# Performance work log

Hardware: AMD Instinct MI355X
Metric: run time of the kernel (lower is better)

## Reference

```python
import jax, jax.numpy as jnp
import numpy as np

WS = 8       # window size
NH = 8       # num heads (c_=256 -> head_dim=32)
BN_EPS = 1e-5
LN_EPS = 1e-5


def _rel_pos_index(ws):
    coords = np.stack(np.meshgrid(np.arange(ws), np.arange(ws), indexing='ij')).reshape(2, -1)
    rel = (coords[:, :, None] - coords[:, None, :]).transpose(1, 2, 0)
    rel[:, :, 0] += ws - 1
    rel[:, :, 1] += ws - 1
    rel[:, :, 0] *= 2 * ws - 1
    return rel.sum(-1)  # (ws*ws, ws*ws) int

RPI = _rel_pos_index(WS)


def _attn_mask(H, W, ws, shift):
    # SW-MSA attention mask, computed from static shapes (numpy)
    img = np.zeros((H, W))
    cnt = 0
    for h in (slice(0, -ws), slice(-ws, -shift), slice(-shift, None)):
        for w in (slice(0, -ws), slice(-ws, -shift), slice(-shift, None)):
            img[h, w] = cnt
            cnt += 1
    mw = img.reshape(H // ws, ws, W // ws, ws).transpose(0, 2, 1, 3).reshape(-1, ws * ws)
    m = mw[:, None, :] - mw[:, :, None]
    return jnp.asarray(np.where(m != 0, -100.0, 0.0).astype(np.float32))  # (nW, N, N)


def _cbs(x, w, bn):
    # 1x1 conv (bias=False) + BatchNorm2d(eval) + SiLU; x:(B,Cin,H,W), w:(Cout,Cin,1,1)
    y = jnp.einsum('bchw,oc->bohw', x, w[:, :, 0, 0])
    g, b, mu, var = bn
    s = g / jnp.sqrt(var + BN_EPS)
    y = y * s[None, :, None, None] + (b - mu * s)[None, :, None, None]
    return y * jax.nn.sigmoid(y)


def _ln(x, g, b):
    mu = x.mean(-1, keepdims=True)
    var = ((x - mu) ** 2).mean(-1, keepdims=True)
    return (x - mu) / jnp.sqrt(var + LN_EPS) * g + b


def _window_attn(x, mask, qkvw, qkvb, pw, pb, rpb):
    B_, N, C = x.shape
    hd = C // NH
    qkv = (x @ qkvw.T + qkvb).reshape(B_, N, 3, NH, hd).transpose(2, 0, 3, 1, 4)
    q, k, v = qkv[0] * (hd ** -0.5), qkv[1], qkv[2]
    attn = jnp.einsum('bhnd,bhmd->bhnm', q, k)  # (B_, NH, N, N)
    bias = rpb[RPI.reshape(-1)].reshape(N, N, NH).transpose(2, 0, 1)
    attn = attn + bias[None]
    if mask is not None:
        nW = mask.shape[0]
        attn = (attn.reshape(B_ // nW, nW, NH, N, N) + mask[None, :, None]).reshape(B_, NH, N, N)
    attn = jax.nn.softmax(attn, axis=-1)
    out = jnp.einsum('bhnm,bhmd->bhnd', attn, v).transpose(0, 2, 1, 3).reshape(B_, N, C)
    return out @ pw.T + pb


def _swin_layer(x, shift, n1g, n1b, qkvw, qkvb, pw, pb, rpb, n2g, n2b, f1w, f1b, f2w, f2b):
    B, C, H, W = x.shape  # H, W divisible by WS (no pad branch)
    shortcut = x.transpose(0, 2, 3, 1).reshape(B, H * W, C)
    xn = _ln(shortcut, n1g, n1b).reshape(B, H, W, C)
    if shift > 0:
        xn = jnp.roll(xn, (-shift, -shift), axis=(1, 2))
        mask = _attn_mask(H, W, WS, shift)
    else:
        mask = None
    nh, nw = H // WS, W // WS
    xw = xn.reshape(B, nh, WS, nw, WS, C).transpose(0, 1, 3, 2, 4, 5).reshape(-1, WS * WS, C)
    aw = _window_attn(xw, mask, qkvw, qkvb, pw, pb, rpb)
    xr = aw.reshape(B, nh, nw, WS, WS, C).transpose(0, 1, 3, 2, 4, 5).reshape(B, H, W, C)
    if shift > 0:
        xr = jnp.roll(xr, (shift, shift), axis=(1, 2))
    x1 = shortcut + xr.reshape(B, H * W, C)
    h = jax.nn.gelu(_ln(x1, n2g, n2b) @ f1w.T + f1b, approximate=False)
    x2 = x1 + (h @ f2w.T + f2b)
    return x2.reshape(B, H, W, C).transpose(0, 3, 1, 2)


def setup_inputs() -> dict:
    key = jax.random.key(0)
    ks = iter(jax.random.split(key, 48))
    C1, C2, C_, NL = 512, 512, 256, 2

    def randn(shape, s=0.02):
        return jax.random.normal(next(ks), shape, jnp.float32) * s

    def bn(c):
        g = jax.random.uniform(next(ks), (c,), jnp.float32, 0.5, 1.5)
        b = randn((c,), 0.1)
        mu = randn((c,), 0.1)
        var = jax.random.uniform(next(ks), (c,), jnp.float32, 0.5, 1.5)
        return jnp.stack([g, b, mu, var])

    return dict(
        x=jax.random.normal(next(ks), (16, C1, 64, 64), jnp.float32),
        cv1_w=randn((C_, C1, 1, 1)), cv1_bn=bn(C_),
        cv2_w=randn((C_, C1, 1, 1)), cv2_bn=bn(C_),
        cv3_w=randn((C2, 2 * C_, 1, 1)), cv3_bn=bn(C2),
        norm1_g=jnp.ones((NL, C_)), norm1_b=jnp.zeros((NL, C_)),
        qkv_w=randn((NL, 3 * C_, C_)), qkv_b=jnp.zeros((NL, 3 * C_)),
        proj_w=randn((NL, C_, C_)), proj_b=jnp.zeros((NL, C_)),
        rpb=randn((NL, (2 * WS - 1) ** 2, NH)),
        norm2_g=jnp.ones((NL, C_)), norm2_b=jnp.zeros((NL, C_)),
        fc1_w=randn((NL, 4 * C_, C_)), fc1_b=jnp.zeros((NL, 4 * C_)),
        fc2_w=randn((NL, C_, 4 * C_)), fc2_b=jnp.zeros((NL, C_)),
    )


def reference(x, cv1_w, cv1_bn, cv2_w, cv2_bn, cv3_w, cv3_bn,
              norm1_g, norm1_b, qkv_w, qkv_b, proj_w, proj_b, rpb,
              norm2_g, norm2_b, fc1_w, fc1_b, fc2_w, fc2_b):
    y = _cbs(x, cv1_w, cv1_bn)
    for i in range(qkv_w.shape[0]):  # n swin layers (alternating W-MSA / SW-MSA)
        shift = 0 if i % 2 == 0 else WS // 2
        y = _swin_layer(y, shift, norm1_g[i], norm1_b[i], qkv_w[i], qkv_b[i],
                        proj_w[i], proj_b[i], rpb[i], norm2_g[i], norm2_b[i],
                        fc1_w[i], fc1_b[i], fc2_w[i], fc2_b[i])
    y2 = _cbs(x, cv2_w, cv2_bn)
    return _cbs(jnp.concatenate([y, y2], axis=1), cv3_w, cv3_bn)
```

## Files before the change

### kernel.cpp

```cpp
#include <hip/hip_runtime.h>
#include <math.h>

using bf16x8 = __attribute__((ext_vector_type(8))) short;
using f32x4  = __attribute__((ext_vector_type(4))) float;
typedef unsigned short u16;

#define DI __device__ __forceinline__

DI u16 f2bf(float f){
  union { float f; unsigned u; } v; v.f = f;
  return (u16)((v.u + 0x7fffu + ((v.u >> 16) & 1u)) >> 16);
}

DI void gll16(const void* g, void* l){
  __builtin_amdgcn_global_load_lds((const __attribute__((address_space(1))) void*)g,
                                   (__attribute__((address_space(3))) void*)l, 16, 0, 0);
}

__global__ void k_cvt(const float* __restrict__ in, u16* __restrict__ out, int n4){
  int i = blockIdx.x * 256 + threadIdx.x;
  if (i >= n4) return;
  float4 v = ((const float4*)in)[i];
  short4 o;
  o.x = (short)f2bf(v.x); o.y = (short)f2bf(v.y);
  o.z = (short)f2bf(v.z); o.w = (short)f2bf(v.w);
  ((short4*)out)[i] = o;
}

__global__ void k_xpose(const float* __restrict__ x, u16* __restrict__ xT){
  __shared__ float tile[64][65];
  int hw0 = blockIdx.x * 64, c0 = blockIdx.y * 64, b = blockIdx.z;
  int tid = threadIdx.x;
  const float* src = x + ((size_t)(b * 512 + c0)) * 4096 + hw0;
  for (int rep = 0; rep < 16; rep++){
    int idx = rep * 256 + tid;
    int cc = idx >> 6, th = idx & 63;
    tile[cc][th] = src[(size_t)cc * 4096 + th];
  }
  __syncthreads();
  u16* dst = xT + ((size_t)(b * 4096 + hw0)) * 512 + c0;
  for (int rep = 0; rep < 16; rep++){
    int idx = rep * 256 + tid;
    int tt = idx >> 6, cc = idx & 63;
    dst[(size_t)tt * 512 + cc] = f2bf(tile[cc][tt]);
  }
}

__global__ void k_ln(const float* __restrict__ xin, const float* __restrict__ g,
                     const float* __restrict__ bta, u16* __restrict__ out){
  int t = blockIdx.x * 4 + (threadIdx.x >> 6);
  int lane = threadIdx.x & 63;
  float4 v = ((const float4*)(xin + (size_t)t * 256))[lane];
  float s  = v.x + v.y + v.z + v.w;
  float s2 = v.x*v.x + v.y*v.y + v.z*v.z + v.w*v.w;
  for (int m = 1; m < 64; m <<= 1){ s += __shfl_xor(s, m, 64); s2 += __shfl_xor(s2, m, 64); }
  float mu  = s * (1.0f/256.0f);
  float var = s2 * (1.0f/256.0f) - mu*mu;
  float inv = rsqrtf(var + 1e-5f);
  float4 gg = ((const float4*)g)[lane];
  float4 bb = ((const float4*)bta)[lane];
  short4 o;
  o.x = (short)f2bf((v.x - mu) * inv * gg.x + bb.x);
  o.y = (short)f2bf((v.y - mu) * inv * gg.y + bb.y);
  o.z = (short)f2bf((v.z - mu) * inv * gg.z + bb.z);
  o.w = (short)f2bf((v.w - mu) * inv * gg.w + bb.w);
  ((short4*)(out + (size_t)t * 256))[lane] = o;
}

struct GemmP {
  const u16* A; const u16* A2; const u16* W;
  int K; int N;
  const float* bias;
  int bnN;
  const float* resid; int ldR;
  float* outF; int ldF;
  u16* outB; int ldB; int colB;
};

template<int MODE>
__launch_bounds__(256)
__global__ void k_gemm(GemmP p){
  __shared__ __align__(16) u16 sA[128 * 64];
  __shared__ __align__(16) u16 sB[128 * 64];
  __shared__ float sT[(MODE == 6) ? 32 * 136 : 1];
  int tid = threadIdx.x;
  int wave = tid >> 6, lane = tid & 63;
  int fq = lane >> 4, fr = lane & 15;
  int m0 = blockIdx.x * 128, n0 = blockIdx.y * 128;
  int wm = (wave >> 1) * 64, wn = (wave & 1) * 64;
  const int K = p.K;

  int rsub = lane >> 3;
  int gk   = ((lane & 7) ^ rsub) << 3;

  f32x4 acc[4][4];
  f32x4 z4 = {0.f, 0.f, 0.f, 0.f};
  #pragma unroll
  for (int i = 0; i < 4; i++)
    #pragma unroll
    for (int j = 0; j < 4; j++) acc[i][j] = z4;

  for (int k0 = 0; k0 < K; k0 += 64){
    #pragma unroll
    for (int it = 0; it < 4; it++){
      int row = (it * 4 + wave) * 8 + rsub;
      const u16* ga;
      if constexpr (MODE == 6){
        const u16* base = (k0 < 256) ? p.A : p.A2;
        ga = base + (size_t)(m0 + row) * 256 + (k0 & 255) + gk;
      } else {
        ga = p.A + (size_t)(m0 + row) * K + k0 + gk;
      }
      gll16(ga, sA + (it * 4 + wave) * 512);
      const u16* gb = p.W + (size_t)(n0 + row) * K + k0 + gk;
      gll16(gb, sB + (it * 4 + wave) * 512);
    }
    __syncthreads();
    #pragma unroll
    for (int kk = 0; kk < 2; kk++){
      bf16x8 af[4], bfr[4];
      #pragma unroll
      for (int i = 0; i < 4; i++){
        int r = wm + i * 16 + fr;
        af[i] = *(const bf16x8*)(sA + r * 64 + ((((kk << 2) + fq) ^ (fr & 7)) << 3));
      }
      #pragma unroll
      for (int j = 0; j < 4; j++){
        int r = wn + j * 16 + fr;
        bfr[j] = *(const bf16x8*)(sB + r * 64 + ((((kk << 2) + fq) ^ (fr & 7)) << 3));
      }
      #pragma unroll
      for (int i = 0; i < 4; i++)
        #pragma unroll
        for (int j = 0; j < 4; j++)
          acc[i][j] = __builtin_amdgcn_mfma_f32_16x16x32_bf16(af[i], bfr[j], acc[i][j], 0, 0, 0);
    }
    __syncthreads();
  }

  if constexpr (MODE != 6){
    #pragma unroll
    for (int j = 0; j < 4; j++){
      int col = n0 + wn + j * 16 + fr;
      float sc = 0.f, sh = 0.f;
      if constexpr (MODE == 0 || MODE == 1){
        float gg = p.bias[col];
        float bb = p.bias[p.bnN + col];
        float mv = p.bias[2 * p.bnN + col];
        float vv = p.bias[3 * p.bnN + col];
        sc = gg * rsqrtf(vv + 1e-5f);
        sh = bb - mv * sc;
      } else {
        sh = p.bias[col];
      }
      #pragma unroll
      for (int i = 0; i < 4; i++){
        #pragma unroll
        for (int rr = 0; rr < 4; rr++){
          int row = m0 + wm + i * 16 + fq * 4 + rr;
          float v = acc[i][j][rr];
          if constexpr (MODE == 0 || MODE == 1){ v = v * sc + sh; v = v / (1.f + __expf(-v)); }
          else v += sh;
          if constexpr (MODE == 3 || MODE == 5) v += p.resid[(size_t)row * p.ldR + col];
          if constexpr (MODE == 4) v = 0.5f * v * (1.f + erff(v * 0.70710678118f));
          if constexpr (MODE == 0 || MODE == 3 || MODE == 5) p.outF[(size_t)row * p.ldF + col] = v;
          if constexpr (MODE == 1 || MODE == 2 || MODE == 4 || MODE == 5)
            p.outB[(size_t)row * p.ldB + p.colB + col] = f2bf(v);
        }
      }
    }
  } else {
    int b = m0 >> 12;
    int hw0 = m0 & 4095;
    #pragma unroll
    for (int ps = 0; ps < 4; ps++){
      if (wn == (ps >> 1) * 64){
        #pragma unroll
        for (int jj = 0; jj < 2; jj++){
          int j = (ps & 1) * 2 + jj;
          int col = n0 + wn + j * 16 + fr;
          float gg = p.bias[col];
          float bb = p.bias[p.bnN + col];
          float mv = p.bias[2 * p.bnN + col];
          float vv = p.bias[3 * p.bnN + col];
          float sc = gg * rsqrtf(vv + 1e-5f);
          float sh = bb - mv * sc;
          int nl = wn + j * 16 + fr - ps * 32;
          #pragma unroll
          for (int i = 0; i < 4; i++)
            #pragma unroll
            for (int rr = 0; rr < 4; rr++){
              float v = acc[i][j][rr];
              v = v * sc + sh; v = v / (1.f + __expf(-v));
              sT[nl * 136 + wm + i * 16 + fq * 4 + rr] = v;
            }
        }
      }
      __syncthreads();
      for (int rep = 0; rep < 16; rep++){
        int flat = rep * 256 + tid;
        int nl = flat >> 7, ml = flat & 127;
        int c = n0 + ps * 32 + nl;
        p.outF[((size_t)(b * 512 + c)) * 4096 + hw0 + ml] = sT[nl * 136 + ml];
      }
      __syncthreads();
    }
  }
}

template<int SHIFT>
__launch_bounds__(256)
__global__ void k_attn(const u16* __restrict__ qkv, const float* __restrict__ rpb,
                       u16* __restrict__ out){
  __shared__ int tmap[64];
  __shared__ float bias_s[1800];
  __shared__ __align__(16) u16 p_s[4][64][72];
  __shared__ __align__(16) u16 vT_s[4][32][72];
  int tid = threadIdx.x, wave = tid >> 6, lane = tid & 63;
  int fq = lane >> 4, fr = lane & 15;
  int wi = blockIdx.x;
  int b = wi >> 6, wh = (wi >> 3) & 7, ww = wi & 7;

  for (int i = tid; i < 1800; i += 256) bias_s[i] = rpb[i];
  if (tid < 64){
    int r = tid >> 3, c = tid & 7;
    int h = (wh * 8 + r + SHIFT) & 63;
    int w = (ww * 8 + c + SHIFT) & 63;
    tmap[tid] = (b << 12) | (h << 6) | w;
  }
  __syncthreads();

  const float scl = 0.17677669529663687f;
  for (int hh = 0; hh < 2; hh++){
    int head = wave * 2 + hh;

    {
      const u16* vrow = qkv + (size_t)tmap[lane] * 768 + 512 + head * 32;
      #pragma unroll
      for (int cg = 0; cg < 4; cg++){
        bf16x8 vv = *(const bf16x8*)(vrow + cg * 8);
        #pragma unroll
        for (int e = 0; e < 8; e++) vT_s[wave][cg * 8 + e][lane] = (u16)vv[e];
      }
    }

    bf16x8 qf[4], kf[4];
    #pragma unroll
    for (int i = 0; i < 4; i++){
      int n = i * 16 + fr;
      size_t base = (size_t)tmap[n] * 768 + head * 32 + fq * 8;
      qf[i] = *(const bf16x8*)(qkv + base);
      kf[i] = *(const bf16x8*)(qkv + base + 256);
    }
    f32x4 z4 = {0.f, 0.f, 0.f, 0.f};
    f32x4 sfr[4][4];
    #pragma unroll
    for (int i = 0; i < 4; i++)
      #pragma unroll
      for (int j = 0; j < 4; j++) sfr[i][j] = z4;
    #pragma unroll
    for (int i = 0; i < 4; i++)
      #pragma unroll
      for (int j = 0; j < 4; j++)
        sfr[i][j] = __builtin_amdgcn_mfma_f32_16x16x32_bf16(qf[i], kf[j], sfr[i][j], 0, 0, 0);

    #pragma unroll
    for (int i = 0; i < 4; i++){
      #pragma unroll
      for (int rr = 0; rr < 4; rr++){
        int rq = i * 16 + fq * 4 + rr;
        int prq = rq >> 3, pcq = rq & 7;
        int idq = 0;
        if (SHIFT > 0){
          int rh = (wh == 7) ? ((prq >= 4) ? 2 : 1) : 0;
          int rw = (ww == 7) ? ((pcq >= 4) ? 2 : 1) : 0;
          idq = rh * 3 + rw;
        }
        float vv[4];
        float mx = -1e30f;
        #pragma unroll
        for (int j = 0; j < 4; j++){
          int m = j * 16 + fr;
          int prk = m >> 3, pck = m & 7;
          float bi = bias_s[((prq - prk + 7) * 15 + (pcq - pck + 7)) * 8 + head];
          float v = sfr[i][j][rr] * scl + bi;
          if (SHIFT > 0){
            int rhk = (wh == 7) ? ((prk >= 4) ? 2 : 1) : 0;
            int rwk = (ww == 7) ? ((pck >= 4) ? 2 : 1) : 0;
            if (idq != rhk * 3 + rwk) v -= 100.f;
          }
          vv[j] = v;
          mx = fmaxf(mx, v);
        }
        for (int mm = 1; mm < 16; mm <<= 1) mx = fmaxf(mx, __shfl_xor(mx, mm, 64));
        float sum = 0.f;
        #pragma unroll
        for (int j = 0; j < 4; j++){ vv[j] = __expf(vv[j] - mx); sum += vv[j]; }
        for (int mm = 1; mm < 16; mm <<= 1) sum += __shfl_xor(sum, mm, 64);
        float inv = 1.0f / sum;
        #pragma unroll
        for (int j = 0; j < 4; j++) p_s[wave][rq][j * 16 + fr] = f2bf(vv[j] * inv);
      }
    }
    __syncthreads();

    f32x4 o[4][2];
    #pragma unroll
    for (int i = 0; i < 4; i++){ o[i][0] = z4; o[i][1] = z4; }
    #pragma unroll
    for (int ks = 0; ks < 2; ks++){
      bf16x8 pa[4], vb[2];
      #pragma unroll
      for (int i = 0; i < 4; i++) pa[i] = *(const bf16x8*)&p_s[wave][i * 16 + fr][ks * 32 + fq * 8];
      #pragma unroll
      for (int j = 0; j < 2; j++) vb[j] = *(const bf16x8*)&vT_s[wave][j * 16 + fr][ks * 32 + fq * 8];
      #pragma unroll
      for (int i = 0; i < 4; i++)
        #pragma unroll
        for (int j = 0; j < 2; j++)
          o[i][j] = __builtin_amdgcn_mfma_f32_16x16x32_bf16(pa[i], vb[j], o[i][j], 0, 0, 0);
    }
    #pragma unroll
    for (int i = 0; i < 4; i++)
      #pragma unroll
      for (int j = 0; j < 2; j++)
        #pragma unroll
        for (int rr = 0; rr < 4; rr++){
          int rq = i * 16 + fq * 4 + rr;
          int t = tmap[rq];
          out[(size_t)t * 256 + head * 32 + j * 16 + fr] = f2bf(o[i][j][rr]);
        }
    __syncthreads();
  }
}

extern "C" void kernel_launch(void* const* d_in, const int* in_sizes, int n_in,
                              void* d_out, int out_size, void* d_ws, size_t ws_size,
                              hipStream_t stream){
  (void)in_sizes; (void)n_in; (void)out_size; (void)ws_size;
  const float* x      = (const float*)d_in[0];
  const float* cv1_w  = (const float*)d_in[1];
  const float* cv1_bn = (const float*)d_in[2];
  const float* cv2_w  = (const float*)d_in[3];
  const float* cv2_bn = (const float*)d_in[4];
  const float* cv3_w  = (const float*)d_in[5];
  const float* cv3_bn = (const float*)d_in[6];
  const float* n1g = (const float*)d_in[7];
  const float* n1b = (const float*)d_in[8];
  const float* qkvw = (const float*)d_in[9];
  const float* qkvb = (const float*)d_in[10];
  const float* pw  = (const float*)d_in[11];
  const float* pb  = (const float*)d_in[12];
  const float* rpb = (const float*)d_in[13];
  const float* n2g = (const float*)d_in[14];
  const float* n2b = (const float*)d_in[15];
  const float* f1w = (const float*)d_in[16];
  const float* f1b = (const float*)d_in[17];
  const float* f2w = (const float*)d_in[18];
  const float* f2b = (const float*)d_in[19];

  char* ws = (char*)d_ws;
  const size_t MB = 1024 * 1024;
  u16*   xT   = (u16*)(ws);
  u16*   ln_o = (u16*)(ws);
  u16*   yF   = (u16*)(ws);
  u16*   at_o = (u16*)(ws + 32 * MB);
  u16*   qkvB = (u16*)(ws + 64 * MB);
  u16*   hB   = qkvB;
  float* yS   = (float*)(ws + 192 * MB);
  float* x1   = (float*)(ws + 256 * MB);
  u16*   wp   = (u16*)(ws + 320 * MB);
  u16*   y2   = (u16*)(ws + 328 * MB);

  u16* wCv1 = wp;
  u16* wCv2 = wp + 131072;
  u16* wCv3 = wp + 262144;
  u16* wQkv = wp + 524288;
  u16* wPrj = wp + 917504;
  u16* wF1  = wp + 1048576;
  u16* wF2  = wp + 1572864;

  auto cvt = [&](const float* src, u16* dst, int n){
    int n4 = n >> 2;
    k_cvt<<<(n4 + 255) / 256, 256, 0, stream>>>(src, dst, n4);
  };
  cvt(cv1_w, wCv1, 131072);
  cvt(cv2_w, wCv2, 131072);
  cvt(cv3_w, wCv3, 262144);
  cvt(qkvw,  wQkv, 393216);
  cvt(pw,    wPrj, 131072);
  cvt(f1w,   wF1,  524288);
  cvt(f2w,   wF2,  524288);

  k_xpose<<<dim3(64, 8, 16), 256, 0, stream>>>(x, xT);

  const int M = 65536;
  auto gemm = [&](int mode, const u16* A, const u16* A2, const u16* W, int K, int N,
                  const float* bias, int bnN, const float* resid, int ldR,
                  float* outF, int ldF, u16* outB, int ldB, int colB){
    GemmP p{A, A2, W, K, N, bias, bnN, resid, ldR, outF, ldF, outB, ldB, colB};
    dim3 g(M / 128, N / 128);
    switch (mode){
      case 0: k_gemm<0><<<g, 256, 0, stream>>>(p); break;
      case 1: k_gemm<1><<<g, 256, 0, stream>>>(p); break;
      case 2: k_gemm<2><<<g, 256, 0, stream>>>(p); break;
      case 3: k_gemm<3><<<g, 256, 0, stream>>>(p); break;
      case 4: k_gemm<4><<<g, 256, 0, stream>>>(p); break;
      case 5: k_gemm<5><<<g, 256, 0, stream>>>(p); break;
      case 6: k_gemm<6><<<g, 256, 0, stream>>>(p); break;
    }
  };

  gemm(0, xT, nullptr, wCv1, 512, 256, cv1_bn, 256, nullptr, 0, yS, 256, nullptr, 0, 0);
  gemm(1, xT, nullptr, wCv2, 512, 256, cv2_bn, 256, nullptr, 0, nullptr, 0, y2, 256, 0);

  for (int l = 0; l < 2; l++){
    k_ln<<<16384, 256, 0, stream>>>(yS, n1g + l * 256, n1b + l * 256, ln_o);
    gemm(2, ln_o, nullptr, wQkv + l * 196608, 256, 768, qkvb + l * 768, 0, nullptr, 0,
         nullptr, 0, qkvB, 768, 0);
    if (l == 0) k_attn<0><<<1024, 256, 0, stream>>>(qkvB, rpb, at_o);
    else        k_attn<4><<<1024, 256, 0, stream>>>(qkvB, rpb + 1800, at_o);
    gemm(3, at_o, nullptr, wPrj + l * 65536, 256, 256, pb + l * 256, 0, yS, 256,
         x1, 256, nullptr, 0, 0);
    k_ln<<<16384, 256, 0, stream>>>(x1, n2g + l * 256, n2b + l * 256, ln_o);
    gemm(4, ln_o, nullptr, wF1 + l * 262144, 256, 1024, f1b + l * 1024, 0, nullptr, 0,
         nullptr, 0, hB, 1024, 0);
    if (l == 0)
      gemm(3, hB, nullptr, wF2 + l * 262144, 1024, 256, f2b + l * 256, 0, x1, 256,
           yS, 256, nullptr, 0, 0);
    else
      gemm(5, hB, nullptr, wF2 + l * 262144, 1024, 256, f2b + l * 256, 0, x1, 256,
           yS, 256, yF, 256, 0);
  }

  gemm(6, yF, y2, wCv3, 512, 512, cv3_bn, 512, nullptr, 0,
       (float*)d_out, 0, nullptr, 0, 0);
}
```

Measured before the change: 1.409 ms.

## Double-buffer GEMM LDS tiles and remap workgroups across XCDs

The GEMM kernel now uses two LDS buffers, so the next K-tile's global loads are issued while MFMAs run on the current tile. Explicit vmcnt waits and raw barriers replace __syncthreads. The 2D grid becomes a 1D grid with an XCD-aware block-id remap that places neighbouring tiles on the same XCD for L2 reuse. This doubles LDS use (64KB per block), which may lower occupancy.

```diff
diff --git a/kernel.cpp b/kernel.cpp
--- a/kernel.cpp
+++ b/kernel.cpp
@@ -69,7 +69,7 @@
 
 struct GemmP {
   const u16* A; const u16* A2; const u16* W;
-  int K; int N;
+  int K; int N; int NB;
   const float* bias;
   int bnN;
   const float* resid; int ldR;
@@ -80,27 +80,25 @@
 template<int MODE>
 __launch_bounds__(256)
 __global__ void k_gemm(GemmP p){
-  __shared__ __align__(16) u16 sA[128 * 64];
-  __shared__ __align__(16) u16 sB[128 * 64];
+  __shared__ __align__(16) u16 sA[2][128 * 64];
+  __shared__ __align__(16) u16 sB[2][128 * 64];
   __shared__ float sT[(MODE == 6) ? 32 * 136 : 1];
   int tid = threadIdx.x;
   int wave = tid >> 6, lane = tid & 63;
   int fq = lane >> 4, fr = lane & 15;
-  int m0 = blockIdx.x * 128, n0 = blockIdx.y * 128;
+
+  int nwg = gridDim.x;
+  int bid = blockIdx.x;
+  int lid = (bid & 7) * (nwg >> 3) + (bid >> 3);
+  int m0 = (lid / p.NB) * 128, n0 = (lid % p.NB) * 128;
+
   int wm = (wave >> 1) * 64, wn = (wave & 1) * 64;
   const int K = p.K;
 
   int rsub = lane >> 3;
   int gk   = ((lane & 7) ^ rsub) << 3;
 
-  f32x4 acc[4][4];
-  f32x4 z4 = {0.f, 0.f, 0.f, 0.f};
-  #pragma unroll
-  for (int i = 0; i < 4; i++)
-    #pragma unroll
-    for (int j = 0; j < 4; j++) acc[i][j] = z4;
-
-  for (int k0 = 0; k0 < K; k0 += 64){
+  auto STAGE = [&](int k0, int c){
     #pragma unroll
     for (int it = 0; it < 4; it++){
       int row = (it * 4 + wave) * 8 + rsub;
@@ -111,23 +109,38 @@
       } else {
         ga = p.A + (size_t)(m0 + row) * K + k0 + gk;
       }
-      gll16(ga, sA + (it * 4 + wave) * 512);
-      const u16* gb = p.W + (size_t)(n0 + row) * K + k0 + gk;
-      gll16(gb, sB + (it * 4 + wave) * 512);
-    }
-    __syncthreads();
+      gll16(ga, &sA[c][(it * 4 + wave) * 512]);
+      gll16(p.W + (size_t)(n0 + row) * K + k0 + gk, &sB[c][(it * 4 + wave) * 512]);
+    }
+  };
+
+  f32x4 acc[4][4];
+  f32x4 z4 = {0.f, 0.f, 0.f, 0.f};
+  #pragma unroll
+  for (int i = 0; i < 4; i++)
+    #pragma unroll
+    for (int j = 0; j < 4; j++) acc[i][j] = z4;
+
+  STAGE(0, 0);
+  int c = 0;
+  for (int k0 = 0; k0 < K; k0 += 64){
+    bool last = (k0 + 64 >= K);
+    if (!last) STAGE(k0 + 64, c ^ 1);
+    if (last) asm volatile("s_waitcnt vmcnt(0)" ::: "memory");
+    else      asm volatile("s_waitcnt vmcnt(8)" ::: "memory");
+    __builtin_amdgcn_s_barrier();
     #pragma unroll
     for (int kk = 0; kk < 2; kk++){
       bf16x8 af[4], bfr[4];
       #pragma unroll
       for (int i = 0; i < 4; i++){
         int r = wm + i * 16 + fr;
-        af[i] = *(const bf16x8*)(sA + r * 64 + ((((kk << 2) + fq) ^ (fr & 7)) << 3));
+        af[i] = *(const bf16x8*)(&sA[c][r * 64 + ((((kk << 2) + fq) ^ (fr & 7)) << 3)]);
       }
       #pragma unroll
       for (int j = 0; j < 4; j++){
         int r = wn + j * 16 + fr;
-        bfr[j] = *(const bf16x8*)(sB + r * 64 + ((((kk << 2) + fq) ^ (fr & 7)) << 3));
+        bfr[j] = *(const bf16x8*)(&sB[c][r * 64 + ((((kk << 2) + fq) ^ (fr & 7)) << 3)]);
       }
       #pragma unroll
       for (int i = 0; i < 4; i++)
@@ -135,7 +148,8 @@
         for (int j = 0; j < 4; j++)
           acc[i][j] = __builtin_amdgcn_mfma_f32_16x16x32_bf16(af[i], bfr[j], acc[i][j], 0, 0, 0);
     }
-    __syncthreads();
+    __builtin_amdgcn_s_barrier();
+    c ^= 1;
   }
 
   if constexpr (MODE != 6){
@@ -200,8 +214,8 @@
       for (int rep = 0; rep < 16; rep++){
         int flat = rep * 256 + tid;
         int nl = flat >> 7, ml = flat & 127;
-        int c = n0 + ps * 32 + nl;
-        p.outF[((size_t)(b * 512 + c)) * 4096 + hw0 + ml] = sT[nl * 136 + ml];
+        int cch = n0 + ps * 32 + nl;
+        p.outF[((size_t)(b * 512 + cch)) * 4096 + hw0 + ml] = sT[nl * 136 + ml];
       }
       __syncthreads();
     }
@@ -398,16 +412,17 @@
   auto gemm = [&](int mode, const u16* A, const u16* A2, const u16* W, int K, int N,
                   const float* bias, int bnN, const float* resid, int ldR,
                   float* outF, int ldF, u16* outB, int ldB, int colB){
-    GemmP p{A, A2, W, K, N, bias, bnN, resid, ldR, outF, ldF, outB, ldB, colB};
-    dim3 g(M / 128, N / 128);
+    int NB = N / 128;
+    GemmP p{A, A2, W, K, N, NB, bias, bnN, resid, ldR, outF, ldF, outB, ldB, colB};
+    int nwg = (M / 128) * NB;
     switch (mode){
-      case 0: k_gemm<0><<<g, 256, 0, stream>>>(p); break;
-      case 1: k_gemm<1><<<g, 256, 0, stream>>>(p); break;
-      case 2: k_gemm<2><<<g, 256, 0, stream>>>(p); break;
-      case 3: k_gemm<3><<<g, 256, 0, stream>>>(p); break;
-      case 4: k_gemm<4><<<g, 256, 0, stream>>>(p); break;
-      case 5: k_gemm<5><<<g, 256, 0, stream>>>(p); break;
-      case 6: k_gemm<6><<<g, 256, 0, stream>>>(p); break;
+      case 0: k_gemm<0><<<nwg, 256, 0, stream>>>(p); break;
+      case 1: k_gemm<1><<<nwg, 256, 0, stream>>>(p); break;
+      case 2: k_gemm<2><<<nwg, 256, 0, stream>>>(p); break;
+      case 3: k_gemm<3><<<nwg, 256, 0, stream>>>(p); break;
+      case 4: k_gemm<4><<<nwg, 256, 0, stream>>>(p); break;
+      case 5: k_gemm<5><<<nwg, 256, 0, stream>>>(p); break;
+      case 6: k_gemm<6><<<nwg, 256, 0, stream>>>(p); break;
     }
   };
 
```

Measured after the change: 1.327 ms. 1.06x faster.
